# Performance work log

Measured on AMD Instinct MI355X. Metric: run time of the kernel, lower is better.

Reference implementation:

```python
import jax, jax.numpy as jnp
import numpy as np

# Dims: B=batch, T=seq, D=input=256=F*F, H=hidden=256=F*F, F=16 factor, R=16 TT rank, 4 gates (I,F,G,O)
F, R, NG = 16, 16, 4


def setup_inputs():
    key = jax.random.key(0)
    ks = jax.random.split(key, 11)
    s = 0.1  # core init scale keeps gate pre-activations O(1)
    inp = {
        "x": jax.random.normal(ks[0], (64, 1024, 256), jnp.float32),
        # TT cores for the 4 input-to-hidden gates (boundary ranks squeezed)
        "ih_g0": s * jax.random.normal(ks[1], (NG, F, R), jnp.float32),
        "ih_g1": s * jax.random.normal(ks[2], (NG, R, F, R), jnp.float32),
        "ih_g2": s * jax.random.normal(ks[3], (NG, R, F, R), jnp.float32),
        "ih_g3": s * jax.random.normal(ks[4], (NG, R, F), jnp.float32),
        "ih_bias": jnp.zeros((NG, F * F), jnp.float32),
        # TT cores for the 4 hidden-to-hidden gates
        "hh_g0": s * jax.random.normal(ks[5], (NG, F, R), jnp.float32),
        "hh_g1": s * jax.random.normal(ks[6], (NG, R, F, R), jnp.float32),
        "hh_g2": s * jax.random.normal(ks[7], (NG, R, F, R), jnp.float32),
        "hh_g3": s * jax.random.normal(ks[8], (NG, R, F), jnp.float32),
        "hh_bias": jnp.zeros((NG, F * F), jnp.float32),
    }
    return inp


def tt_linear(x2, g0, g1, g2, g3, bias):
    # x2: [N, F*F] -> contract TT cores per gate g -> [N, NG, F*F]
    n = x2.shape[0]
    x3 = x2.reshape(n, F, F)
    t = jnp.einsum('bmn,gmr->bgnr', x3, g0)      # contract first input factor
    t = jnp.einsum('bgnr,grns->bgs', t, g1)      # contract second input factor
    t = jnp.einsum('bgs,gsot->bgot', t, g2)      # emit first output factor
    y = jnp.einsum('bgot,gtp->bgop', t, g3)      # emit second output factor
    return y.reshape(n, NG, F * F) + bias        # bias: [NG, F*F]


def reference(x, ih_g0, ih_g1, ih_g2, ih_g3, ih_bias,
              hh_g0, hh_g1, hh_g2, hh_g3, hh_bias):
    B, T, D = x.shape
    H = F * F
    # Precompute input-to-hidden gate contributions for all timesteps at once
    ih_all = tt_linear(x.reshape(B * T, D), ih_g0, ih_g1, ih_g2, ih_g3, ih_bias)
    ih_all = ih_all.reshape(B, T, NG, H).transpose(1, 0, 2, 3)  # [T,B,4,H]

    def step(carry, ih_t):
        h, c = carry
        gates = ih_t + tt_linear(h, hh_g0, hh_g1, hh_g2, hh_g3, hh_bias)
        i = jax.nn.sigmoid(gates[:, 0])
        f = jax.nn.sigmoid(gates[:, 1])
        g = jnp.tanh(gates[:, 2])
        o = jax.nn.sigmoid(gates[:, 3])
        c = f * c + i * g
        h = o * jnp.tanh(c)
        return (h, c), h

    h0 = jnp.zeros((B, H), x.dtype)
    c0 = jnp.zeros((B, H), x.dtype)
    (h, c), ys = jax.lax.scan(step, (h0, c0), ih_all)
    output = ys.transpose(1, 0, 2)  # [B,T,H]
    return output, (h, c)
```

## Files before the change

kernel.cpp:

```cpp
#include <hip/hip_runtime.h>


#define WS_A1I 0
#define WS_A1H 16384
#define WS_C2I 32768
#define WS_C2H 49152
#define WS_BIAS 65536
#define WS_T2 66560

__device__ __forceinline__ void bar_lds() {
    asm volatile("s_waitcnt lgkmcnt(0)\n\ts_barrier" ::: "memory");
}

template <int CTRL>
__device__ __forceinline__ float dpp_add(float v) {
    int s = __builtin_amdgcn_update_dpp(0, __float_as_int(v), CTRL, 0xF, 0xF, true);
    return v + __int_as_float(s);
}
template <int CTRL>
__device__ __forceinline__ float dpp_bcast(float v) {
    int s = __builtin_amdgcn_update_dpp(0, __float_as_int(v), CTRL, 0xF, 0xF, true);
    return __int_as_float(s);
}

__global__ void k_compose(const float* __restrict__ g0i, const float* __restrict__ g1i,
                          const float* __restrict__ g2i, const float* __restrict__ g3i,
                          const float* __restrict__ bi,
                          const float* __restrict__ g0h, const float* __restrict__ g1h,
                          const float* __restrict__ g2h, const float* __restrict__ g3h,
                          const float* __restrict__ bh,
                          float* __restrict__ ws) {
    int id = blockIdx.x * 256 + threadIdx.x;
    if (id < 16384) {
        int g = id >> 12, s = (id >> 8) & 15, mn = id & 255;
        int m = mn >> 4, n = mn & 15;
        float aI = 0.f, aH = 0.f;
        for (int r = 0; r < 16; ++r) {
            aI += g0i[(g * 16 + m) * 16 + r] * g1i[((g * 16 + r) * 16 + n) * 16 + s];
            aH += g0h[(g * 16 + m) * 16 + r] * g1h[((g * 16 + r) * 16 + n) * 16 + s];
        }
        ws[WS_A1I + (g * 16 + s) * 256 + mn] = aI;
        ws[WS_A1H + (g * 16 + s) * 256 + mn] = aH;
    } else if (id < 32768) {
        int id2 = id - 16384;
        int g = id2 >> 12, s = (id2 >> 8) & 15, j = id2 & 255;
        int o = j >> 4, p = j & 15;
        float aI = 0.f, aH = 0.f;
        for (int t = 0; t < 16; ++t) {
            aI += g2i[((g * 16 + s) * 16 + o) * 16 + t] * g3i[(g * 16 + t) * 16 + p];
            aH += g2h[((g * 16 + s) * 16 + o) * 16 + t] * g3h[(g * 16 + t) * 16 + p];
        }
        ws[WS_C2I + (g * 16 + s) * 256 + j] = aI;
        ws[WS_C2H + (g * 16 + s) * 256 + j] = aH;
    } else if (id < 33792) {
        int id2 = id - 32768;
        ws[WS_BIAS + id2] = bi[id2] + bh[id2];
    }
}

__global__ __launch_bounds__(256, 2) void k_t2ih(const float* __restrict__ x,
                                                 const float* __restrict__ ws,
                                                 float* __restrict__ T2) {
    __shared__ __align__(16) float Xs[64 * 256];
    __shared__ __align__(16) float As[64 * 256];
    const int tid = threadIdx.x;
    const long r0 = (long)blockIdx.x * 64;

    const float4* X4 = (const float4*)(x + r0 * 256);
    const float4* A4 = (const float4*)(ws + WS_A1I);
    float4* Xs4 = (float4*)Xs;
    float4* As4 = (float4*)As;
#pragma unroll
    for (int k = 0; k < 16; ++k) {
        int idx = tid + k * 256;
        int row = idx >> 6, c = idx & 63;
        int sw = (row << 6) | (c ^ (row & 15));
        Xs4[sw] = X4[idx];
        As4[sw] = A4[idx];
    }
    __syncthreads();

    const int ro = tid & 15;
    const int q  = tid >> 4;
    float acc[4][4];
#pragma unroll
    for (int i = 0; i < 4; ++i)
#pragma unroll
        for (int j = 0; j < 4; ++j) acc[i][j] = 0.f;

    for (int mn4 = 0; mn4 < 64; ++mn4) {
        float4 a[4], xv[4];
#pragma unroll
        for (int j = 0; j < 4; ++j) {
            int row = ro * 4 + j;
            a[j] = As4[(row << 6) | (mn4 ^ (row & 15))];
        }
#pragma unroll
        for (int i = 0; i < 4; ++i) {
            int row = q * 4 + i;
            xv[i] = Xs4[(row << 6) | (mn4 ^ (row & 15))];
        }
#pragma unroll
        for (int i = 0; i < 4; ++i)
#pragma unroll
            for (int j = 0; j < 4; ++j)
                acc[i][j] += xv[i].x * a[j].x + xv[i].y * a[j].y +
                             xv[i].z * a[j].z + xv[i].w * a[j].w;
    }
#pragma unroll
    for (int i = 0; i < 4; ++i)
#pragma unroll
        for (int j = 0; j < 4; ++j)
            T2[(r0 + q * 4 + i) * 64 + ro * 4 + j] = acc[i][j];
}

__global__ __launch_bounds__(1024, 4) void k_lstm(const float* __restrict__ ws,
                                                  const float* __restrict__ T2,
                                                  float* __restrict__ out) {
    __shared__ __align__(16) float hS[256];
    __shared__ __align__(16) float t2hS[64];
    __shared__ __align__(16) float t2iS[2][64];

    const int tid  = threadIdx.x;
    const int w    = tid >> 6;
    const int lane = tid & 63;
    const int b    = blockIdx.x;

    const int uab = 4 * w + (lane >> 4);
    const int sub = lane & 15;
    float a1r[16];
    {
        const float4* A1h4 = (const float4*)(ws + WS_A1H);
#pragma unroll
        for (int kk = 0; kk < 4; ++kk) {
            float4 v = A1h4[uab * 64 + sub * 4 + kk];
            a1r[4 * kk + 0] = v.x; a1r[4 * kk + 1] = v.y;
            a1r[4 * kk + 2] = v.z; a1r[4 * kk + 3] = v.w;
        }
    }

    const int jj = lane >> 2;
    const int g  = lane & 3;
    const int j  = 16 * w + jj;
    float c2h[16], c2i[16];
#pragma unroll
    for (int s = 0; s < 16; ++s) {
        c2h[s] = ws[WS_C2H + (16 * g + s) * 256 + j];
        c2i[s] = ws[WS_C2I + (16 * g + s) * 256 + j];
    }
    float bias = ws[WS_BIAS + g * 256 + j];
    const float am = (g == 2) ? 2.0f : 1.0f;
    const float as = 1.442695040888963f * am;

#pragma unroll
    for (int i = 0; i < 16; ++i)
        asm volatile("" : "+v"(a1r[i]), "+v"(c2h[i]), "+v"(c2i[i]));

    const int hw = ((jj >> 2) << 6) + (w << 2) + (jj & 3);

    float c = 0.f, h_last = 0.f;
    if (tid < 256) hS[tid] = 0.f;
    const float* T2b = T2 + (long)b * 1024 * 64;
    const float4* T2b4 = (const float4*)T2b;
    float4 preA = make_float4(0.f, 0.f, 0.f, 0.f);
    float4 preB = make_float4(0.f, 0.f, 0.f, 0.f);
    if (tid < 16) {
        ((float4*)t2iS[0])[tid] = T2b4[tid];
        preA = T2b4[16 + tid];
    }
    bar_lds();

    float* outB = out + (long)b * 1024 * 256;
    const float4* hS4 = (const float4*)hS;
    const float4* th4 = (const float4*)t2hS;

    auto body = [&](int t, float4& preW, float4& preL) {
        float4 s4 = make_float4(0.f, 0.f, 0.f, 0.f);
#pragma unroll
        for (int kk = 0; kk < 4; ++kk) {
            float4 hv = hS4[kk * 16 + sub];
            s4.x += hv.x * a1r[4 * kk + 0];
            s4.y += hv.y * a1r[4 * kk + 1];
            s4.z += hv.z * a1r[4 * kk + 2];
            s4.w += hv.w * a1r[4 * kk + 3];
        }
        float tv = (s4.x + s4.y) + (s4.z + s4.w);
        if ((tid < 16) && (t + 1 < 1024))
            ((float4*)t2iS[(t + 1) & 1])[tid] = preW;
        if ((tid < 16) && (t + 2 < 1024))
            preL = T2b4[(t + 2) * 16 + tid];
        tv = dpp_add<0x111>(tv);
        tv = dpp_add<0x112>(tv);
        tv = dpp_add<0x114>(tv);
        tv = dpp_add<0x118>(tv);
        if (sub == 15) t2hS[uab] = tv;

        bar_lds();

        const float4* ti4 = (const float4*)t2iS[t & 1];
        float acc = bias;
#pragma unroll
        for (int q = 0; q < 4; ++q) {
            float4 th = th4[g * 4 + q];
            float4 ti = ti4[g * 4 + q];
            acc += th.x * c2h[4*q+0] + th.y * c2h[4*q+1] + th.z * c2h[4*q+2] + th.w * c2h[4*q+3]
                 + ti.x * c2i[4*q+0] + ti.y * c2i[4*q+1] + ti.z * c2i[4*q+2] + ti.w * c2i[4*q+3];
        }
        float e   = __builtin_amdgcn_exp2f(as * acc);
        float act = 1.0f - am * __builtin_amdgcn_rcpf(1.0f + e);
        float gi = dpp_bcast<0x00>(act);
        float gf = dpp_bcast<0x55>(act);
        float gg = dpp_bcast<0xAA>(act);
        float go = dpp_bcast<0xFF>(act);
        c = gf * c + gi * gg;
        float e2 = __builtin_amdgcn_exp2f(2.885390081777926f * c);
        float th_ = 1.0f - 2.0f * __builtin_amdgcn_rcpf(1.0f + e2);
        float h = go * th_;
        h_last = h;
        if (g == 0) {
            hS[hw] = h;
            outB[t * 256 + j] = h;
        }

        bar_lds();
    };

    for (int t = 0; t < 1024; t += 2) {
        body(t, preA, preB);
        body(t + 1, preB, preA);
    }

    if (g == 0) {
        out[16777216 + b * 256 + j] = h_last;
        out[16777216 + 16384 + b * 256 + j] = c;
    }
}

extern "C" void kernel_launch(void* const* d_in, const int* in_sizes, int n_in,
                              void* d_out, int out_size, void* d_ws, size_t ws_size,
                              hipStream_t stream) {
    const float* x     = (const float*)d_in[0];
    const float* ih_g0 = (const float*)d_in[1];
    const float* ih_g1 = (const float*)d_in[2];
    const float* ih_g2 = (const float*)d_in[3];
    const float* ih_g3 = (const float*)d_in[4];
    const float* ih_b  = (const float*)d_in[5];
    const float* hh_g0 = (const float*)d_in[6];
    const float* hh_g1 = (const float*)d_in[7];
    const float* hh_g2 = (const float*)d_in[8];
    const float* hh_g3 = (const float*)d_in[9];
    const float* hh_b  = (const float*)d_in[10];
    float* out = (float*)d_out;
    float* ws  = (float*)d_ws;

    k_compose<<<132, 256, 0, stream>>>(ih_g0, ih_g1, ih_g2, ih_g3, ih_b,
                                       hh_g0, hh_g1, hh_g2, hh_g3, hh_b, ws);
    k_t2ih<<<1024, 256, 0, stream>>>(x, ws, ws + WS_T2);
    k_lstm<<<64, 1024, 0, stream>>>(ws, ws + WS_T2, out);
}
```

Baseline: 919.9 us.

## Use packed FMA in projection and recurrence, split projection K into halves

Replaces the scalar multiply-add chains in both the input-projection kernel and the LSTM recurrence with v_pk_fma_f32 on float pairs, halving instruction count for the dot products. The projection kernel now stages the K dimension in two halves with half-size LDS tiles and a new swizzle, which reduces shared memory per block and may allow more resident blocks. It also adds an extra sync pair per block and changes the summation order, so float rounding differs slightly.

```diff
diff --git a/kernel.cpp b/kernel.cpp
--- a/kernel.cpp
+++ b/kernel.cpp
@@ -7,6 +7,14 @@
 #define WS_C2H 49152
 #define WS_BIAS 65536
 #define WS_T2 66560
+
+typedef float v2f __attribute__((ext_vector_type(2)));
+
+__device__ __forceinline__ v2f pk_fma(v2f a, v2f b, v2f c) {
+    v2f d;
+    asm("v_pk_fma_f32 %0, %1, %2, %3" : "=v"(d) : "v"(a), "v"(b), "v"(c));
+    return d;
+}
 
 __device__ __forceinline__ void bar_lds() {
     asm volatile("s_waitcnt lgkmcnt(0)\n\ts_barrier" ::: "memory");
@@ -61,57 +69,65 @@
 __global__ __launch_bounds__(256, 2) void k_t2ih(const float* __restrict__ x,
                                                  const float* __restrict__ ws,
                                                  float* __restrict__ T2) {
-    __shared__ __align__(16) float Xs[64 * 256];
-    __shared__ __align__(16) float As[64 * 256];
+    __shared__ __align__(16) float Xs[64 * 128];
+    __shared__ __align__(16) float As[64 * 128];
     const int tid = threadIdx.x;
     const long r0 = (long)blockIdx.x * 64;
-
-    const float4* X4 = (const float4*)(x + r0 * 256);
-    const float4* A4 = (const float4*)(ws + WS_A1I);
+    const int ro = tid & 15;
+    const int q  = tid >> 4;
+
+    const float4* X4g = (const float4*)x;
+    const float4* A4  = (const float4*)(ws + WS_A1I);
     float4* Xs4 = (float4*)Xs;
     float4* As4 = (float4*)As;
-#pragma unroll
-    for (int k = 0; k < 16; ++k) {
-        int idx = tid + k * 256;
-        int row = idx >> 6, c = idx & 63;
-        int sw = (row << 6) | (c ^ (row & 15));
-        Xs4[sw] = X4[idx];
-        As4[sw] = A4[idx];
-    }
-    __syncthreads();
-
-    const int ro = tid & 15;
-    const int q  = tid >> 4;
-    float acc[4][4];
+
+    v2f acc2[4][4];
 #pragma unroll
     for (int i = 0; i < 4; ++i)
 #pragma unroll
-        for (int j = 0; j < 4; ++j) acc[i][j] = 0.f;
-
-    for (int mn4 = 0; mn4 < 64; ++mn4) {
-        float4 a[4], xv[4];
-#pragma unroll
-        for (int j = 0; j < 4; ++j) {
-            int row = ro * 4 + j;
-            a[j] = As4[(row << 6) | (mn4 ^ (row & 15))];
-        }
-#pragma unroll
-        for (int i = 0; i < 4; ++i) {
-            int row = q * 4 + i;
-            xv[i] = Xs4[(row << 6) | (mn4 ^ (row & 15))];
-        }
-#pragma unroll
-        for (int i = 0; i < 4; ++i)
-#pragma unroll
-            for (int j = 0; j < 4; ++j)
-                acc[i][j] += xv[i].x * a[j].x + xv[i].y * a[j].y +
-                             xv[i].z * a[j].z + xv[i].w * a[j].w;
+        for (int j = 0; j < 4; ++j) acc2[i][j] = (v2f){0.f, 0.f};
+
+    for (int half = 0; half < 2; ++half) {
+        __syncthreads();
+#pragma unroll
+        for (int k = 0; k < 8; ++k) {
+            int idx = k * 256 + tid;
+            int row = idx >> 5, c = idx & 31;
+            int sw = (row << 5) | (c ^ ((row >> 2) & 15));
+            Xs4[sw] = X4g[(r0 + row) * 64 + half * 32 + c];
+            As4[sw] = A4[row * 64 + half * 32 + c];
+        }
+        __syncthreads();
+
+#pragma unroll 4
+        for (int mn4 = 0; mn4 < 32; ++mn4) {
+            float4 a[4], xv[4];
+#pragma unroll
+            for (int j = 0; j < 4; ++j) {
+                int row = ro * 4 + j;
+                a[j] = As4[(row << 5) | (mn4 ^ ro)];
+            }
+#pragma unroll
+            for (int i = 0; i < 4; ++i) {
+                int row = q * 4 + i;
+                xv[i] = Xs4[(row << 5) | (mn4 ^ q)];
+            }
+#pragma unroll
+            for (int i = 0; i < 4; ++i)
+#pragma unroll
+                for (int j = 0; j < 4; ++j) {
+                    acc2[i][j] = pk_fma((v2f){xv[i].x, xv[i].y},
+                                        (v2f){a[j].x, a[j].y}, acc2[i][j]);
+                    acc2[i][j] = pk_fma((v2f){xv[i].z, xv[i].w},
+                                        (v2f){a[j].z, a[j].w}, acc2[i][j]);
+                }
+        }
     }
 #pragma unroll
     for (int i = 0; i < 4; ++i)
 #pragma unroll
         for (int j = 0; j < 4; ++j)
-            T2[(r0 + q * 4 + i) * 64 + ro * 4 + j] = acc[i][j];
+            T2[(r0 + q * 4 + i) * 64 + ro * 4 + j] = acc2[i][j].x + acc2[i][j].y;
 }
 
 __global__ __launch_bounds__(1024, 4) void k_lstm(const float* __restrict__ ws,
@@ -128,33 +144,43 @@
 
     const int uab = 4 * w + (lane >> 4);
     const int sub = lane & 15;
-    float a1r[16];
+    v2f a1p[8];
     {
         const float4* A1h4 = (const float4*)(ws + WS_A1H);
 #pragma unroll
         for (int kk = 0; kk < 4; ++kk) {
             float4 v = A1h4[uab * 64 + sub * 4 + kk];
-            a1r[4 * kk + 0] = v.x; a1r[4 * kk + 1] = v.y;
-            a1r[4 * kk + 2] = v.z; a1r[4 * kk + 3] = v.w;
+            a1p[2 * kk + 0] = (v2f){v.x, v.y};
+            a1p[2 * kk + 1] = (v2f){v.z, v.w};
         }
     }
 
     const int jj = lane >> 2;
     const int g  = lane & 3;
     const int j  = 16 * w + jj;
-    float c2h[16], c2i[16];
-#pragma unroll
-    for (int s = 0; s < 16; ++s) {
-        c2h[s] = ws[WS_C2H + (16 * g + s) * 256 + j];
-        c2i[s] = ws[WS_C2I + (16 * g + s) * 256 + j];
+    v2f c2hp[8], c2ip[8];
+#pragma unroll
+    for (int qq = 0; qq < 4; ++qq) {
+        float h0 = ws[WS_C2H + (16 * g + 4 * qq + 0) * 256 + j];
+        float h1 = ws[WS_C2H + (16 * g + 4 * qq + 1) * 256 + j];
+        float h2 = ws[WS_C2H + (16 * g + 4 * qq + 2) * 256 + j];
+        float h3 = ws[WS_C2H + (16 * g + 4 * qq + 3) * 256 + j];
+        float i0 = ws[WS_C2I + (16 * g + 4 * qq + 0) * 256 + j];
+        float i1 = ws[WS_C2I + (16 * g + 4 * qq + 1) * 256 + j];
+        float i2 = ws[WS_C2I + (16 * g + 4 * qq + 2) * 256 + j];
+        float i3 = ws[WS_C2I + (16 * g + 4 * qq + 3) * 256 + j];
+        c2hp[2 * qq + 0] = (v2f){h0, h1};
+        c2hp[2 * qq + 1] = (v2f){h2, h3};
+        c2ip[2 * qq + 0] = (v2f){i0, i1};
+        c2ip[2 * qq + 1] = (v2f){i2, i3};
     }
     float bias = ws[WS_BIAS + g * 256 + j];
     const float am = (g == 2) ? 2.0f : 1.0f;
     const float as = 1.442695040888963f * am;
 
 #pragma unroll
-    for (int i = 0; i < 16; ++i)
-        asm volatile("" : "+v"(a1r[i]), "+v"(c2h[i]), "+v"(c2i[i]));
+    for (int i = 0; i < 8; ++i)
+        asm volatile("" : "+v"(a1p[i]), "+v"(c2hp[i]), "+v"(c2ip[i]));
 
     const int hw = ((jj >> 2) << 6) + (w << 2) + (jj & 3);
 
@@ -175,16 +201,14 @@
     const float4* th4 = (const float4*)t2hS;
 
     auto body = [&](int t, float4& preW, float4& preL) {
-        float4 s4 = make_float4(0.f, 0.f, 0.f, 0.f);
+        v2f sA = (v2f){0.f, 0.f}, sB = (v2f){0.f, 0.f};
 #pragma unroll
         for (int kk = 0; kk < 4; ++kk) {
             float4 hv = hS4[kk * 16 + sub];
-            s4.x += hv.x * a1r[4 * kk + 0];
-            s4.y += hv.y * a1r[4 * kk + 1];
-            s4.z += hv.z * a1r[4 * kk + 2];
-            s4.w += hv.w * a1r[4 * kk + 3];
-        }
-        float tv = (s4.x + s4.y) + (s4.z + s4.w);
+            sA = pk_fma((v2f){hv.x, hv.y}, a1p[2 * kk + 0], sA);
+            sB = pk_fma((v2f){hv.z, hv.w}, a1p[2 * kk + 1], sB);
+        }
+        float tv = (sA.x + sA.y) + (sB.x + sB.y);
         if ((tid < 16) && (t + 1 < 1024))
             ((float4*)t2iS[(t + 1) & 1])[tid] = preW;
         if ((tid < 16) && (t + 2 < 1024))
@@ -198,14 +222,17 @@
         bar_lds();
 
         const float4* ti4 = (const float4*)t2iS[t & 1];
-        float acc = bias;
-#pragma unroll
-        for (int q = 0; q < 4; ++q) {
-            float4 th = th4[g * 4 + q];
-            float4 ti = ti4[g * 4 + q];
-            acc += th.x * c2h[4*q+0] + th.y * c2h[4*q+1] + th.z * c2h[4*q+2] + th.w * c2h[4*q+3]
-                 + ti.x * c2i[4*q+0] + ti.y * c2i[4*q+1] + ti.z * c2i[4*q+2] + ti.w * c2i[4*q+3];
-        }
+        v2f aH = (v2f){bias, 0.f}, aL = (v2f){0.f, 0.f};
+#pragma unroll
+        for (int qq = 0; qq < 4; ++qq) {
+            float4 th = th4[g * 4 + qq];
+            float4 ti = ti4[g * 4 + qq];
+            aH = pk_fma((v2f){th.x, th.y}, c2hp[2 * qq + 0], aH);
+            aL = pk_fma((v2f){th.z, th.w}, c2hp[2 * qq + 1], aL);
+            aH = pk_fma((v2f){ti.x, ti.y}, c2ip[2 * qq + 0], aH);
+            aL = pk_fma((v2f){ti.z, ti.w}, c2ip[2 * qq + 1], aL);
+        }
+        float acc = (aH.x + aH.y) + (aL.x + aL.y);
         float e   = __builtin_amdgcn_exp2f(as * acc);
         float act = 1.0f - am * __builtin_amdgcn_rcpf(1.0f + e);
         float gi = dpp_bcast<0x00>(act);
```

Result: faster. 868.4 us (-5.6%).
